# Kernel tuning notes

Measured on AMD Instinct MI355X. Metric: run time of the kernel, lower is better.

The kernel has to match this reference:

```python
import jax, jax.numpy as jnp
import numpy as np

N_STATIC = 20
N_DYNAMIC = 10
INPUT_DIM = N_STATIC + N_DYNAMIC * 9 + 8  # 118
EMBED = 128
HIDDEN = 1536
HIDDEN2 = 1024
OUT = 128
T = 2048


def setup_inputs() -> dict:
    key = jax.random.key(0)
    ks = jax.random.split(key, 20)
    s = lambda i, shape: jax.random.normal(ks[i], shape, dtype=jnp.float32) * 0.02
    inp = {
        "inputVecs": jax.random.normal(ks[0], (T, INPUT_DIM), dtype=jnp.float32),
        # init_hidden(): randn(num_layers, 1, hidden_dim) -> stored as [2, H]
        "h0": jax.random.normal(ks[1], (2, HIDDEN), dtype=jnp.float32),
        "c0": jax.random.normal(ks[2], (2, HIDDEN), dtype=jnp.float32),
        # LSTM layer 0 (input = INPUT_DIM + EMBED)
        "W_ih0": s(3, (4 * HIDDEN, INPUT_DIM + EMBED)),
        "W_hh0": s(4, (4 * HIDDEN, HIDDEN)),
        "b_ih0": s(5, (4 * HIDDEN,)),
        "b_hh0": s(6, (4 * HIDDEN,)),
        # LSTM layer 1
        "W_ih1": s(7, (4 * HIDDEN, HIDDEN)),
        "W_hh1": s(8, (4 * HIDDEN, HIDDEN)),
        "b_ih1": s(9, (4 * HIDDEN,)),
        "b_hh1": s(10, (4 * HIDDEN,)),
        # hiddenLinear: hidden_dim -> hidden2
        "W_hl": s(11, (HIDDEN2, HIDDEN)),
        "b_hl": s(12, (HIDDEN2,)),
        # linear: hidden2 -> output_dim
        "W_out": s(13, (OUT, HIDDEN2)),
        "b_out": s(14, (OUT,)),
        # map: output_dim -> embed_size
        "W_map": s(15, (EMBED, OUT)),
        "b_map": s(16, (EMBED,)),
    }
    return inp


def _lstm_cell(x, h, c, W_ih, W_hh, b_ih, b_hh):
    # torch gate order: i, f, g, o
    gates = W_ih @ x + b_ih + W_hh @ h + b_hh
    i, f, g, o = jnp.split(gates, 4)
    i = jax.nn.sigmoid(i)
    f = jax.nn.sigmoid(f)
    g = jnp.tanh(g)
    o = jax.nn.sigmoid(o)
    c_new = f * c + i * g
    h_new = o * jnp.tanh(c_new)
    return h_new, c_new


def reference(inputVecs, h0, c0, W_ih0, W_hh0, b_ih0, b_hh0,
              W_ih1, W_hh1, b_ih1, b_hh1,
              W_hl, b_hl, W_out, b_out, W_map, b_map):
    embed0 = jnp.zeros((EMBED,), dtype=inputVecs.dtype)

    def step(carry, x):
        h, c, emb = carry  # h,c: [2, H]; emb: [EMBED]
        xt = jnp.concatenate([x, emb])
        h0n, c0n = _lstm_cell(xt, h[0], c[0], W_ih0, W_hh0, b_ih0, b_hh0)
        h1n, c1n = _lstm_cell(h0n, h[1], c[1], W_ih1, W_hh1, b_ih1, b_hh1)
        # dropout p=0 -> identity; two stacked linears (no nonlinearity, faithful)
        y = W_out @ (W_hl @ h1n + b_hl) + b_out
        y = jax.nn.softmax(y)
        emb_new = W_map @ y + b_map
        return (jnp.stack([h0n, h1n]), jnp.stack([c0n, c1n]), emb_new), y

    _, outputs = jax.lax.scan(step, (h0, c0, embed0), inputVecs)
    return outputs  # [T, OUT]
```

## Files before the change

### kernel.cpp

```cpp
#include <hip/hip_runtime.h>
#include <math.h>
#include <stdint.h>

#define T_STEPS 2048
#define XDIM 118
#define EMBD 128
#define HD 1536
#define NA 96
#define NB 128
#define NBLK (NA + NB + 1)

#define EP_A   0
#define EP_B   128
#define EP_C   256
#define EP_AG  288
#define EP_N   320

#define SMEM_BYTES 160032

struct Params {
  const float *x, *h0in, *c0in;
  const float *Wih0, *Whh0, *bih0, *bhh0;
  const float *Wih1, *Whh1, *bih1, *bhh1;
  const float *Whl, *bhl, *Wout, *bout, *Wmap, *bmap;
  float *PRE, *Wc, *bc, *h0buf, *h1buf, *embbuf, *PART;
  uint32_t *ep;
  float *out;
};

__device__ __forceinline__ float bf_lo(uint32_t u){ return __uint_as_float(u << 16); }
__device__ __forceinline__ float bf_hi(uint32_t u){ return __uint_as_float(u & 0xffff0000u); }
__device__ __forceinline__ uint32_t packbf(float a, float b){
  uint32_t ua = __float_as_uint(a), ub = __float_as_uint(b);
  ua = (ua + 0x7fffu + ((ua >> 16) & 1u)) >> 16;
  ub = (ub + 0x7fffu + ((ub >> 16) & 1u)) & 0xffff0000u;
  return (ua & 0xffffu) | ub;
}
__device__ __forceinline__ float gload(const float* p){
  return __hip_atomic_load(p, __ATOMIC_RELAXED, __HIP_MEMORY_SCOPE_AGENT);
}
__device__ __forceinline__ void gstore(float* p, float v){
  __hip_atomic_store(p, v, __ATOMIC_RELAXED, __HIP_MEMORY_SCOPE_AGENT);
}
__device__ __forceinline__ uint32_t gloadu(const uint32_t* p){
  return __hip_atomic_load(p, __ATOMIC_RELAXED, __HIP_MEMORY_SCOPE_AGENT);
}
__device__ __forceinline__ void gstoreu(uint32_t* p, uint32_t v){
  __hip_atomic_store(p, v, __ATOMIC_RELAXED, __HIP_MEMORY_SCOPE_AGENT);
}
__device__ __forceinline__ float sigm(float x){ return 1.f / (1.f + __expf(-x)); }

__device__ __forceinline__ float asrc(const Params& P, int r, int k){
  if (k < HD) return P.Whh0[(size_t)r * HD + k];
  return P.Wih0[(size_t)r * (XDIM + EMBD) + XDIM + (k - HD)];
}
__device__ void run_A(const Params& P, int bid, uint32_t* smem){
  const int tid = threadIdx.x;
  const int w = tid >> 6, l = tid & 63;
  const int O = bid * 16 + w;
  float* xv = (float*)smem;
  uint2* wl2 = (uint2*)(smem + 1664);
  uint32_t wr[4][8];
  uint32_t wremb[4];
#pragma unroll
  for (int g = 0; g < 4; ++g){
    int r = g * HD + O;
#pragma unroll
    for (int p = 0; p < 8; ++p)
      wr[g][p] = packbf(asrc(P, r, 128 * p + 2 * l), asrc(P, r, 128 * p + 2 * l + 1));
#pragma unroll
    for (int q = 0; q < 2; ++q){
      uint2 u;
      u.x = packbf(asrc(P, r, 128 * (8 + 2 * q) + 2 * l), asrc(P, r, 128 * (8 + 2 * q) + 2 * l + 1));
      u.y = packbf(asrc(P, r, 128 * (9 + 2 * q) + 2 * l), asrc(P, r, 128 * (9 + 2 * q) + 2 * l + 1));
      wl2[(q * 4 + g) * 1024 + tid] = u;
    }
    wremb[g] = packbf(asrc(P, r, 1536 + 2 * l), asrc(P, r, 1537 + 2 * l));
  }
  float cst = P.c0in[O];
  int alive = 1;
  __syncthreads();
  for (int t = 0; t < T_STEPS; ++t){
    const float* pre = P.PRE + (size_t)t * 6144;
    float q0 = pre[O], q1 = pre[HD + O], q2 = pre[2 * HD + O], q3 = pre[3 * HD + O];
    if (w == 0 && alive){
      uint32_t n = 0;
      while (gloadu(P.ep + EP_AG) < (uint32_t)t){
        if (++n > 5000000u){ alive = 0; break; }
      }
    }
    __syncthreads();
    const float* hp = P.h0buf + (((t & 1) ^ 1) * HD);
    xv[tid] = gload(hp + tid);
    if (tid < 512) xv[1024 + tid] = gload(hp + 1024 + tid);
    __syncthreads();
    float a0 = 0.f, a1 = 0.f, a2 = 0.f, a3 = 0.f;
#pragma unroll
    for (int p = 0; p < 8; ++p){
      float2 x2 = *(const float2*)&xv[128 * p + 2 * l];
      uint32_t u0 = wr[0][p], u1 = wr[1][p], u2 = wr[2][p], u3 = wr[3][p];
      a0 += bf_lo(u0) * x2.x + bf_hi(u0) * x2.y;
      a1 += bf_lo(u1) * x2.x + bf_hi(u1) * x2.y;
      a2 += bf_lo(u2) * x2.x + bf_hi(u2) * x2.y;
      a3 += bf_lo(u3) * x2.x + bf_hi(u3) * x2.y;
    }
#pragma unroll
    for (int q = 0; q < 2; ++q){
      float2 xa = *(const float2*)&xv[128 * (8 + 2 * q) + 2 * l];
      float2 xb = *(const float2*)&xv[128 * (9 + 2 * q) + 2 * l];
      uint2 u0 = wl2[(q * 4 + 0) * 1024 + tid];
      uint2 u1 = wl2[(q * 4 + 1) * 1024 + tid];
      uint2 u2 = wl2[(q * 4 + 2) * 1024 + tid];
      uint2 u3 = wl2[(q * 4 + 3) * 1024 + tid];
      a0 += bf_lo(u0.x) * xa.x + bf_hi(u0.x) * xa.y + bf_lo(u0.y) * xb.x + bf_hi(u0.y) * xb.y;
      a1 += bf_lo(u1.x) * xa.x + bf_hi(u1.x) * xa.y + bf_lo(u1.y) * xb.x + bf_hi(u1.y) * xb.y;
      a2 += bf_lo(u2.x) * xa.x + bf_hi(u2.x) * xa.y + bf_lo(u2.y) * xb.x + bf_hi(u2.y) * xb.y;
      a3 += bf_lo(u3.x) * xa.x + bf_hi(u3.x) * xa.y + bf_lo(u3.y) * xb.x + bf_hi(u3.y) * xb.y;
    }
    if (w == 0 && alive){
      uint32_t n = 0;
      while (gloadu(P.ep + EP_C) < (uint32_t)t){
        if (++n > 5000000u){ alive = 0; break; }
      }
    }
    __syncthreads();
    if (tid < EMBD) xv[HD + tid] = gload(P.embbuf + (((t & 1) ^ 1) * EMBD) + tid);
    __syncthreads();
    {
      float2 x2 = *(const float2*)&xv[1536 + 2 * l];
      a0 += bf_lo(wremb[0]) * x2.x + bf_hi(wremb[0]) * x2.y;
      a1 += bf_lo(wremb[1]) * x2.x + bf_hi(wremb[1]) * x2.y;
      a2 += bf_lo(wremb[2]) * x2.x + bf_hi(wremb[2]) * x2.y;
      a3 += bf_lo(wremb[3]) * x2.x + bf_hi(wremb[3]) * x2.y;
    }
#pragma unroll
    for (int m = 1; m < 64; m <<= 1){
      a0 += __shfl_xor(a0, m, 64);
      a1 += __shfl_xor(a1, m, 64);
      a2 += __shfl_xor(a2, m, 64);
      a3 += __shfl_xor(a3, m, 64);
    }
    float gi = sigm(a0 + q0);
    float gf = sigm(a1 + q1);
    float gg = tanhf(a2 + q2);
    float go = sigm(a3 + q3);
    cst = gf * cst + gi * gg;
    float hn = go * tanhf(cst);
    if (l == 0) gstore(P.h0buf + (t & 1) * HD + O, hn);
    __syncthreads();
    if (tid == 0) gstoreu(P.ep + EP_A + bid, (uint32_t)(t + 1));
  }
}

__device__ __forceinline__ float bsrc(const Params& P, int r, int k){
  if (k < HD) return P.Wih1[(size_t)r * HD + k];
  return P.Whh1[(size_t)r * HD + (k - HD)];
}
__device__ void run_B(const Params& P, int bidb, uint32_t* smem){
  const int tid = threadIdx.x;
  const int w = tid >> 6, l = tid & 63;
  const int base = bidb * 12;
  float* xv = (float*)smem;
  uint2* wl2 = (uint2*)(smem + 3072);
  float* g1lds = (float*)(smem + 39936);
  float* c1lds = g1lds + 48;
  float* h1lds = c1lds + 12;
  uint32_t wr[3][12];
  float bias[3];
#pragma unroll
  for (int jj = 0; jj < 3; ++jj){
    int idx = 3 * w + jj;
    int g = idx / 12, o = idx % 12;
    int r = g * HD + base + o;
    bias[jj] = P.bih1[r] + P.bhh1[r];
#pragma unroll
    for (int p = 0; p < 12; ++p)
      wr[jj][p] = packbf(bsrc(P, r, 128 * p + 2 * l), bsrc(P, r, 128 * p + 2 * l + 1));
#pragma unroll
    for (int q = 0; q < 6; ++q){
      uint2 u;
      u.x = packbf(bsrc(P, r, 128 * (12 + 2 * q) + 2 * l), bsrc(P, r, 128 * (12 + 2 * q) + 2 * l + 1));
      u.y = packbf(bsrc(P, r, 128 * (13 + 2 * q) + 2 * l), bsrc(P, r, 128 * (13 + 2 * q) + 2 * l + 1));
      wl2[(q * 3 + jj) * 1024 + tid] = u;
    }
  }
  const int jrow = tid >> 2, cpart = tid & 3;
  float wc0 = 0.f, wc1 = 0.f, wc2 = 0.f;
  if (tid < 512){
    const float* wcp = P.Wc + (size_t)jrow * HD + base + cpart * 3;
    wc0 = wcp[0]; wc1 = wcp[1]; wc2 = wcp[2];
  }
  if (tid < 12) c1lds[tid] = P.c0in[HD + base + tid];
  int alive = 1;
  __syncthreads();
  for (int t = 0; t < T_STEPS; ++t){
    if (w == 0 && alive){
      uint32_t n = 0;
      while (gloadu(P.ep + EP_C) < (uint32_t)t){
        if (++n > 5000000u){ alive = 0; break; }
      }
    }
    __syncthreads();
    const float* h1p = P.h1buf + (((t & 1) ^ 1) * HD);
    xv[1536 + tid] = gload(h1p + tid);
    if (tid < 512) xv[2560 + tid] = gload(h1p + 1024 + tid);
    __syncthreads();
    float a0 = 0.f, a1 = 0.f, a2 = 0.f;
#pragma unroll
    for (int q = 0; q < 6; ++q){
      float2 xa = *(const float2*)&xv[128 * (12 + 2 * q) + 2 * l];
      float2 xb = *(const float2*)&xv[128 * (13 + 2 * q) + 2 * l];
      uint2 u0 = wl2[(q * 3 + 0) * 1024 + tid];
      uint2 u1 = wl2[(q * 3 + 1) * 1024 + tid];
      uint2 u2 = wl2[(q * 3 + 2) * 1024 + tid];
      a0 += bf_lo(u0.x) * xa.x + bf_hi(u0.x) * xa.y + bf_lo(u0.y) * xb.x + bf_hi(u0.y) * xb.y;
      a1 += bf_lo(u1.x) * xa.x + bf_hi(u1.x) * xa.y + bf_lo(u1.y) * xb.x + bf_hi(u1.y) * xb.y;
      a2 += bf_lo(u2.x) * xa.x + bf_hi(u2.x) * xa.y + bf_lo(u2.y) * xb.x + bf_hi(u2.y) * xb.y;
    }
    if (w == 0 && alive){
      uint32_t tgt = (uint32_t)(t + 1), n = 0;
      if (bidb == 0){
        while (1){
          uint32_t v0 = gloadu(P.ep + EP_A + l);
          uint32_t v1 = (l < 32) ? gloadu(P.ep + EP_A + 64 + l) : tgt;
          if (__all(v0 >= tgt && v1 >= tgt)) break;
          if (++n > 5000000u){ alive = 0; break; }
        }
        if (l == 0 && alive) gstoreu(P.ep + EP_AG, tgt);
      } else {
        while (gloadu(P.ep + EP_AG) < tgt){
          if (++n > 5000000u){ alive = 0; break; }
        }
      }
    }
    __syncthreads();
    const float* h0p = P.h0buf + (t & 1) * HD;
    xv[tid] = gload(h0p + tid);
    if (tid < 512) xv[1024 + tid] = gload(h0p + 1024 + tid);
    __syncthreads();
#pragma unroll
    for (int p = 0; p < 12; ++p){
      float2 x2 = *(const float2*)&xv[128 * p + 2 * l];
      uint32_t u0 = wr[0][p], u1 = wr[1][p], u2 = wr[2][p];
      a0 += bf_lo(u0) * x2.x + bf_hi(u0) * x2.y;
      a1 += bf_lo(u1) * x2.x + bf_hi(u1) * x2.y;
      a2 += bf_lo(u2) * x2.x + bf_hi(u2) * x2.y;
    }
#pragma unroll
    for (int m = 1; m < 64; m <<= 1){
      a0 += __shfl_xor(a0, m, 64);
      a1 += __shfl_xor(a1, m, 64);
      a2 += __shfl_xor(a2, m, 64);
    }
    if (l == 0){
      g1lds[3 * w + 0] = a0 + bias[0];
      g1lds[3 * w + 1] = a1 + bias[1];
      g1lds[3 * w + 2] = a2 + bias[2];
    }
    __syncthreads();
    if (tid < 12){
      int o = tid;
      float gi = sigm(g1lds[o]);
      float gf = sigm(g1lds[12 + o]);
      float gg = tanhf(g1lds[24 + o]);
      float go = sigm(g1lds[36 + o]);
      float c = gf * c1lds[o] + gi * gg;
      c1lds[o] = c;
      float hn = go * tanhf(c);
      h1lds[o] = hn;
      gstore(P.h1buf + (t & 1) * HD + base + o, hn);
    }
    __syncthreads();
    if (tid < 512){
      float pp = wc0 * h1lds[cpart * 3] + wc1 * h1lds[cpart * 3 + 1] + wc2 * h1lds[cpart * 3 + 2];
      pp += __shfl_xor(pp, 1, 64);
      pp += __shfl_xor(pp, 2, 64);
      if (cpart == 0) gstore(P.PART + bidb * 128 + jrow, pp);
    }
    __syncthreads();
    if (tid == 0) gstoreu(P.ep + EP_B + bidb, (uint32_t)(t + 1));
  }
}

__device__ void run_C(const Params& P, uint32_t* smem){
  const int tid = threadIdx.x;
  float* partred = (float*)smem;
  float* lg   = (float*)(smem + 1024);
  float* plds = (float*)(smem + 1152);
  float* bcs  = (float*)(smem + 1280);
  float* red2 = (float*)(smem + 1408);
  float wm[16];
  const int e = tid >> 3, jc = tid & 7;
#pragma unroll
  for (int i = 0; i < 16; ++i) wm[i] = P.Wmap[(size_t)e * 128 + jc * 16 + i];
  float bm = P.bmap[e];
  if (tid < 128) bcs[tid] = P.bc[tid];
  int alive = 1;
  const int w = tid >> 6, l = tid & 63;
  __syncthreads();
  for (int t = 0; t < T_STEPS; ++t){
    if (w == 0 && alive){
      uint32_t tgt = (uint32_t)(t + 1), n = 0;
      while (1){
        uint32_t v0 = gloadu(P.ep + EP_B + l);
        uint32_t v1 = gloadu(P.ep + EP_B + 64 + l);
        if (__all(v0 >= tgt && v1 >= tgt)) break;
        if (++n > 5000000u){ alive = 0; break; }
      }
    }
    __syncthreads();
    const int j = tid & 127, b8 = tid >> 7;
    float s = 0.f;
#pragma unroll
    for (int i = 0; i < 16; ++i) s += gload(P.PART + (b8 * 16 + i) * 128 + j);
    partred[b8 * 128 + j] = s;
    __syncthreads();
    if (tid < 128){
      float lt = bcs[tid];
#pragma unroll
      for (int i = 0; i < 8; ++i) lt += partred[i * 128 + tid];
      lg[tid] = lt;
    }
    __syncthreads();
    if (tid < 64){
      float m = fmaxf(lg[tid], lg[tid + 64]);
#pragma unroll
      for (int k = 1; k < 64; k <<= 1) m = fmaxf(m, __shfl_xor(m, k, 64));
      float sd = __expf(lg[tid] - m) + __expf(lg[tid + 64] - m);
#pragma unroll
      for (int k = 1; k < 64; k <<= 1) sd += __shfl_xor(sd, k, 64);
      if (tid == 0){ red2[0] = m; red2[1] = 1.f / sd; }
    }
    __syncthreads();
    if (tid < 128){
      float pv = __expf(lg[tid] - red2[0]) * red2[1];
      plds[tid] = pv;
      P.out[(size_t)t * 128 + tid] = pv;
    }
    __syncthreads();
    float a = 0.f;
#pragma unroll
    for (int i = 0; i < 16; ++i) a += wm[i] * plds[jc * 16 + i];
    a += __shfl_xor(a, 1, 64);
    a += __shfl_xor(a, 2, 64);
    a += __shfl_xor(a, 4, 64);
    if (jc == 0) gstore(P.embbuf + (t & 1) * EMBD + e, a + bm);
    __syncthreads();
    if (tid == 0) gstoreu(P.ep + EP_C, (uint32_t)(t + 1));
  }
}

__global__ __launch_bounds__(1024) void k_lstm(Params P){
  extern __shared__ __align__(16) uint32_t smem[];
  int bid = blockIdx.x;
  if (bid < NA) run_A(P, bid, smem);
  else if (bid < NA + NB) run_B(P, bid - NA, smem);
  else run_C(P, smem);
}

__global__ void k_init(const float* h0in, float* h0buf, float* h1buf, float* embbuf,
                       uint32_t* ep){
  int tid = threadIdx.x;
  for (int i = tid; i < HD; i += 256){
    float a = h0in[i], b = h0in[HD + i];
    h0buf[i] = a; h0buf[HD + i] = a;
    h1buf[i] = b; h1buf[HD + i] = b;
  }
  if (tid < 128){ embbuf[tid] = 0.f; embbuf[128 + tid] = 0.f; }
  for (int i = tid; i < EP_N; i += 256) ep[i] = 0u;
}

__global__ void k_pre(const float* x, const float* Wih0, const float* bih0, const float* bhh0, float* PRE){
  int tb = blockIdx.x >> 2;
  int rc = blockIdx.x & 3;
  int tid = threadIdx.x;
  __shared__ float xl[32 * XDIM];
  for (int i = tid; i < 32 * XDIM; i += 256){
    int tt = i / XDIM, k = i % XDIM;
    xl[i] = x[(size_t)(tb * 32 + tt) * XDIM + k];
  }
  __syncthreads();
  for (int rr = 0; rr < 6; ++rr){
    int r = rc * HD + rr * 256 + tid;
    float acc[32];
#pragma unroll
    for (int t = 0; t < 32; ++t) acc[t] = 0.f;
    const float* wrow = Wih0 + (size_t)r * (XDIM + EMBD);
    for (int k = 0; k < XDIM; ++k){
      float wv = wrow[k];
#pragma unroll
      for (int t = 0; t < 32; ++t) acc[t] += wv * xl[t * XDIM + k];
    }
    float bb = bih0[r] + bhh0[r];
    for (int t = 0; t < 32; ++t)
      PRE[(size_t)(tb * 32 + t) * 6144 + r] = acc[t] + bb;
  }
}

__global__ void k_wc(const float* Whl, const float* Wout, const float* bhl, const float* bout,
                     float* Wc, float* bc){
  if (blockIdx.x == 96){
    int j = threadIdx.x;
    if (j < 128){
      float a = 0.f;
      for (int m = 0; m < 1024; ++m) a += Wout[(size_t)j * 1024 + m] * bhl[m];
      bc[j] = a + bout[j];
    }
    return;
  }
  int kt = blockIdx.x % 6, jt = blockIdx.x / 6;
  __shared__ float wo[8 * 1024];
  int tid = threadIdx.x;
  for (int i = tid; i < 8 * 1024; i += 256) wo[i] = Wout[(size_t)(jt * 8) * 1024 + i];
  __syncthreads();
  int k = kt * 256 + tid;
  float acc[8];
#pragma unroll
  for (int jj = 0; jj < 8; ++jj) acc[jj] = 0.f;
  for (int m = 0; m < 1024; ++m){
    float wl = Whl[(size_t)m * HD + k];
#pragma unroll
    for (int jj = 0; jj < 8; ++jj) acc[jj] += wo[jj * 1024 + m] * wl;
  }
#pragma unroll
  for (int jj = 0; jj < 8; ++jj) Wc[(size_t)(jt * 8 + jj) * HD + k] = acc[jj];
}

__global__ void k_sentinel(float* out){ out[0] = 1.0e6f; }

extern "C" void kernel_launch(void* const* d_in, const int* in_sizes, int n_in,
                              void* d_out, int out_size, void* d_ws, size_t ws_size,
                              hipStream_t stream){
  (void)in_sizes; (void)n_in; (void)out_size;
  const float* x    = (const float*)d_in[0];
  const float* h0in = (const float*)d_in[1];
  const float* c0in = (const float*)d_in[2];
  const float* Wih0 = (const float*)d_in[3];
  const float* Whh0 = (const float*)d_in[4];
  const float* bih0 = (const float*)d_in[5];
  const float* bhh0 = (const float*)d_in[6];
  const float* Wih1 = (const float*)d_in[7];
  const float* Whh1 = (const float*)d_in[8];
  const float* bih1 = (const float*)d_in[9];
  const float* bhh1 = (const float*)d_in[10];
  const float* Whl  = (const float*)d_in[11];
  const float* bhl  = (const float*)d_in[12];
  const float* Wout = (const float*)d_in[13];
  const float* bout = (const float*)d_in[14];
  const float* Wmap = (const float*)d_in[15];
  const float* bmap = (const float*)d_in[16];
  float* out = (float*)d_out;
  float* ws = (float*)d_ws;

  size_t off = 0;
  float* PRE    = ws + off; off += (size_t)T_STEPS * 6144;
  float* Wc     = ws + off; off += 128 * HD;
  float* bc     = ws + off; off += 128;
  float* h0buf  = ws + off; off += 2 * HD;
  float* h1buf  = ws + off; off += 2 * HD;
  float* embbuf = ws + off; off += 2 * EMBD;
  float* PART   = ws + off; off += 128 * 128;
  off = (off + 63) & ~(size_t)63;
  uint32_t* ep  = (uint32_t*)(ws + off); off += EP_N;

  if (ws_size < off * sizeof(float) + 1024){
    hipLaunchKernelGGL(k_sentinel, dim3(1), dim3(1), 0, stream, out);
    return;
  }

  (void)hipFuncSetAttribute(reinterpret_cast<const void*>(k_lstm),
                            hipFuncAttributeMaxDynamicSharedMemorySize, SMEM_BYTES);

  hipLaunchKernelGGL(k_init, dim3(1), dim3(256), 0, stream, h0in, h0buf, h1buf, embbuf, ep);
  hipLaunchKernelGGL(k_pre, dim3(256), dim3(256), 0, stream, x, Wih0, bih0, bhh0, PRE);
  hipLaunchKernelGGL(k_wc, dim3(97), dim3(256), 0, stream, Whl, Wout, bhl, bout, Wc, bc);

  Params P;
  P.x = x; P.h0in = h0in; P.c0in = c0in;
  P.Wih0 = Wih0; P.Whh0 = Whh0; P.bih0 = bih0; P.bhh0 = bhh0;
  P.Wih1 = Wih1; P.Whh1 = Whh1; P.bih1 = bih1; P.bhh1 = bhh1;
  P.Whl = Whl; P.bhl = bhl; P.Wout = Wout; P.bout = bout; P.Wmap = Wmap; P.bmap = bmap;
  P.PRE = PRE; P.Wc = Wc; P.bc = bc;
  P.h0buf = h0buf; P.h1buf = h1buf; P.embbuf = embbuf; P.PART = PART;
  P.ep = ep; P.out = out;

  hipLaunchKernelGGL(k_lstm, dim3(NBLK), dim3(1024), SMEM_BYTES, stream, P);
}
```

Before: 33.43 ms.

## Fold embedding map into layer-0 weights and replace block barriers with LDS flags

Precomputes Wfold = Wih0_emb·Wmap and bfold = Wih0_emb·bmap, folding bfold into PRE for t>0. Layer-0 blocks can then consume the softmax output y directly, which removes the map matvec and one stage from the serial per-step chain. Intra-block __syncthreads waits are replaced by an LDS flag that wave 0 sets after polling global counters. Layer-0 blocks now poll all EP_A counters themselves instead of relying on an aggregated flag from block B0, and the softmax is done by a single wave. This shortens the per-step critical path, at the cost of extra bf16 rounding in the folded weights and more fragile spin-wait synchronisation.

```diff
diff --git a/kernel.cpp b/kernel.cpp
--- a/kernel.cpp
+++ b/kernel.cpp
@@ -13,17 +13,17 @@
 #define EP_A   0
 #define EP_B   128
 #define EP_C   256
-#define EP_AG  288
 #define EP_N   320
 
-#define SMEM_BYTES 160032
+#define SMEM_BYTES 160048
 
 struct Params {
   const float *x, *h0in, *c0in;
   const float *Wih0, *Whh0, *bih0, *bhh0;
   const float *Wih1, *Whh1, *bih1, *bhh1;
-  const float *Whl, *bhl, *Wout, *bout, *Wmap, *bmap;
-  float *PRE, *Wc, *bc, *h0buf, *h1buf, *embbuf, *PART;
+  const float *Whl, *bhl, *Wout, *bout;
+  const float *Wfold;
+  float *PRE, *Wc, *bc, *h0buf, *h1buf, *ybuf, *PART;
   uint32_t *ep;
   float *out;
 };
@@ -50,6 +50,17 @@
 }
 __device__ __forceinline__ float sigm(float x){ return 1.f / (1.f + __expf(-x)); }
 
+__device__ __forceinline__ void lds_set(volatile uint32_t* f, uint32_t v){
+  asm volatile("" ::: "memory");
+  *f = v;
+  asm volatile("" ::: "memory");
+}
+__device__ __forceinline__ void lds_wait(volatile uint32_t* f, uint32_t tgt){
+  uint32_t n = 0;
+  while (*f < tgt){ if (++n > 1000000000u) break; }
+  asm volatile("" ::: "memory");
+}
+
 __device__ __forceinline__ float asrc(const Params& P, int r, int k){
   if (k < HD) return P.Whh0[(size_t)r * HD + k];
   return P.Wih0[(size_t)r * (XDIM + EMBD) + XDIM + (k - HD)];
@@ -60,8 +71,9 @@
   const int O = bid * 16 + w;
   float* xv = (float*)smem;
   uint2* wl2 = (uint2*)(smem + 1664);
+  volatile uint32_t* flg = smem + 18048;
   uint32_t wr[4][8];
-  uint32_t wremb[4];
+  uint32_t wry[4];
 #pragma unroll
   for (int g = 0; g < 4; ++g){
     int r = g * HD + O;
@@ -75,21 +87,29 @@
       u.y = packbf(asrc(P, r, 128 * (9 + 2 * q) + 2 * l), asrc(P, r, 128 * (9 + 2 * q) + 2 * l + 1));
       wl2[(q * 4 + g) * 1024 + tid] = u;
     }
-    wremb[g] = packbf(asrc(P, r, 1536 + 2 * l), asrc(P, r, 1537 + 2 * l));
+    wry[g] = packbf(P.Wfold[(size_t)r * 128 + 2 * l], P.Wfold[(size_t)r * 128 + 2 * l + 1]);
   }
   float cst = P.c0in[O];
   int alive = 1;
+  if (tid < 2) flg[tid] = 0u;
   __syncthreads();
   for (int t = 0; t < T_STEPS; ++t){
     const float* pre = P.PRE + (size_t)t * 6144;
     float q0 = pre[O], q1 = pre[HD + O], q2 = pre[2 * HD + O], q3 = pre[3 * HD + O];
-    if (w == 0 && alive){
-      uint32_t n = 0;
-      while (gloadu(P.ep + EP_AG) < (uint32_t)t){
-        if (++n > 5000000u){ alive = 0; break; }
-      }
-    }
-    __syncthreads();
+    if (w == 0){
+      if (alive && t > 0){
+        uint32_t n = 0;
+        while (1){
+          uint32_t v0 = gloadu(P.ep + EP_A + l);
+          uint32_t v1 = (l < 32) ? gloadu(P.ep + EP_A + 64 + l) : (uint32_t)t;
+          if (__all(v0 >= (uint32_t)t && v1 >= (uint32_t)t)) break;
+          if (++n > 5000000u){ alive = 0; break; }
+        }
+      }
+      if (l == 0) lds_set(flg + 0, (uint32_t)t);
+    } else {
+      lds_wait(flg + 0, (uint32_t)t);
+    }
     const float* hp = P.h0buf + (((t & 1) ^ 1) * HD);
     xv[tid] = gload(hp + tid);
     if (tid < 512) xv[1024 + tid] = gload(hp + 1024 + tid);
@@ -117,21 +137,24 @@
       a2 += bf_lo(u2.x) * xa.x + bf_hi(u2.x) * xa.y + bf_lo(u2.y) * xb.x + bf_hi(u2.y) * xb.y;
       a3 += bf_lo(u3.x) * xa.x + bf_hi(u3.x) * xa.y + bf_lo(u3.y) * xb.x + bf_hi(u3.y) * xb.y;
     }
-    if (w == 0 && alive){
-      uint32_t n = 0;
-      while (gloadu(P.ep + EP_C) < (uint32_t)t){
-        if (++n > 5000000u){ alive = 0; break; }
-      }
-    }
-    __syncthreads();
-    if (tid < EMBD) xv[HD + tid] = gload(P.embbuf + (((t & 1) ^ 1) * EMBD) + tid);
-    __syncthreads();
+    if (w == 0){
+      if (alive && t > 0){
+        uint32_t n = 0;
+        while (gloadu(P.ep + EP_C) < (uint32_t)t){
+          if (++n > 5000000u){ alive = 0; break; }
+        }
+      }
+      if (l == 0) lds_set(flg + 1, (uint32_t)t);
+    } else {
+      lds_wait(flg + 1, (uint32_t)t);
+    }
     {
-      float2 x2 = *(const float2*)&xv[1536 + 2 * l];
-      a0 += bf_lo(wremb[0]) * x2.x + bf_hi(wremb[0]) * x2.y;
-      a1 += bf_lo(wremb[1]) * x2.x + bf_hi(wremb[1]) * x2.y;
-      a2 += bf_lo(wremb[2]) * x2.x + bf_hi(wremb[2]) * x2.y;
-      a3 += bf_lo(wremb[3]) * x2.x + bf_hi(wremb[3]) * x2.y;
+      const float* yb = P.ybuf + (((t & 1) ^ 1) * EMBD) + 2 * l;
+      float yx = gload(yb), yy = gload(yb + 1);
+      a0 += bf_lo(wry[0]) * yx + bf_hi(wry[0]) * yy;
+      a1 += bf_lo(wry[1]) * yx + bf_hi(wry[1]) * yy;
+      a2 += bf_lo(wry[2]) * yx + bf_hi(wry[2]) * yy;
+      a3 += bf_lo(wry[3]) * yx + bf_hi(wry[3]) * yy;
     }
 #pragma unroll
     for (int m = 1; m < 64; m <<= 1){
@@ -162,9 +185,9 @@
   const int base = bidb * 12;
   float* xv = (float*)smem;
   uint2* wl2 = (uint2*)(smem + 3072);
-  float* g1lds = (float*)(smem + 39936);
-  float* c1lds = g1lds + 48;
-  float* h1lds = c1lds + 12;
+  float* g1 = (float*)(smem + 39936);
+  float* c1 = g1 + 48;
+  volatile uint32_t* flg = smem + 40008;
   uint32_t wr[3][12];
   float bias[3];
 #pragma unroll
@@ -190,17 +213,22 @@
     const float* wcp = P.Wc + (size_t)jrow * HD + base + cpart * 3;
     wc0 = wcp[0]; wc1 = wcp[1]; wc2 = wcp[2];
   }
-  if (tid < 12) c1lds[tid] = P.c0in[HD + base + tid];
+  if (tid < 12) c1[12 + tid] = P.c0in[HD + base + tid];
+  if (tid < 2) flg[tid] = 0u;
   int alive = 1;
   __syncthreads();
   for (int t = 0; t < T_STEPS; ++t){
-    if (w == 0 && alive){
-      uint32_t n = 0;
-      while (gloadu(P.ep + EP_C) < (uint32_t)t){
-        if (++n > 5000000u){ alive = 0; break; }
-      }
-    }
-    __syncthreads();
+    if (w == 0){
+      if (alive && t > 0){
+        uint32_t n = 0;
+        while (gloadu(P.ep + EP_C) < (uint32_t)t){
+          if (++n > 5000000u){ alive = 0; break; }
+        }
+      }
+      if (l == 0) lds_set(flg + 0, (uint32_t)t);
+    } else {
+      lds_wait(flg + 0, (uint32_t)t);
+    }
     const float* h1p = P.h1buf + (((t & 1) ^ 1) * HD);
     xv[1536 + tid] = gload(h1p + tid);
     if (tid < 512) xv[2560 + tid] = gload(h1p + 1024 + tid);
@@ -217,23 +245,21 @@
       a1 += bf_lo(u1.x) * xa.x + bf_hi(u1.x) * xa.y + bf_lo(u1.y) * xb.x + bf_hi(u1.y) * xb.y;
       a2 += bf_lo(u2.x) * xa.x + bf_hi(u2.x) * xa.y + bf_lo(u2.y) * xb.x + bf_hi(u2.y) * xb.y;
     }
-    if (w == 0 && alive){
-      uint32_t tgt = (uint32_t)(t + 1), n = 0;
-      if (bidb == 0){
+    if (w == 0){
+      uint32_t tgt = (uint32_t)(t + 1);
+      if (alive){
+        uint32_t n = 0;
         while (1){
           uint32_t v0 = gloadu(P.ep + EP_A + l);
           uint32_t v1 = (l < 32) ? gloadu(P.ep + EP_A + 64 + l) : tgt;
           if (__all(v0 >= tgt && v1 >= tgt)) break;
           if (++n > 5000000u){ alive = 0; break; }
         }
-        if (l == 0 && alive) gstoreu(P.ep + EP_AG, tgt);
-      } else {
-        while (gloadu(P.ep + EP_AG) < tgt){
-          if (++n > 5000000u){ alive = 0; break; }
-        }
-      }
-    }
-    __syncthreads();
+      }
+      if (l == 0) lds_set(flg + 1, tgt);
+    } else {
+      lds_wait(flg + 1, (uint32_t)(t + 1));
+    }
     const float* h0p = P.h0buf + (t & 1) * HD;
     xv[tid] = gload(h0p + tid);
     if (tid < 512) xv[1024 + tid] = gload(h0p + 1024 + tid);
@@ -253,29 +279,37 @@
       a2 += __shfl_xor(a2, m, 64);
     }
     if (l == 0){
-      g1lds[3 * w + 0] = a0 + bias[0];
-      g1lds[3 * w + 1] = a1 + bias[1];
-      g1lds[3 * w + 2] = a2 + bias[2];
-    }
-    __syncthreads();
-    if (tid < 12){
-      int o = tid;
-      float gi = sigm(g1lds[o]);
-      float gf = sigm(g1lds[12 + o]);
-      float gg = tanhf(g1lds[24 + o]);
-      float go = sigm(g1lds[36 + o]);
-      float c = gf * c1lds[o] + gi * gg;
-      c1lds[o] = c;
-      float hn = go * tanhf(c);
-      h1lds[o] = hn;
-      gstore(P.h1buf + (t & 1) * HD + base + o, hn);
-    }
-    __syncthreads();
+      g1[3 * w + 0] = a0 + bias[0];
+      g1[3 * w + 1] = a1 + bias[1];
+      g1[3 * w + 2] = a2 + bias[2];
+    }
+    __syncthreads();
+    const int par = ((t & 1) ^ 1) * 12, cur = (t & 1) * 12;
     if (tid < 512){
-      float pp = wc0 * h1lds[cpart * 3] + wc1 * h1lds[cpart * 3 + 1] + wc2 * h1lds[cpart * 3 + 2];
+      float h[3], cc[3];
+#pragma unroll
+      for (int ii = 0; ii < 3; ++ii){
+        int o = cpart * 3 + ii;
+        float gi = sigm(g1[o]);
+        float gf = sigm(g1[12 + o]);
+        float gg = tanhf(g1[24 + o]);
+        float go = sigm(g1[36 + o]);
+        float c = gf * c1[par + o] + gi * gg;
+        cc[ii] = c;
+        h[ii] = go * tanhf(c);
+      }
+      float pp = wc0 * h[0] + wc1 * h[1] + wc2 * h[2];
       pp += __shfl_xor(pp, 1, 64);
       pp += __shfl_xor(pp, 2, 64);
       if (cpart == 0) gstore(P.PART + bidb * 128 + jrow, pp);
+      if (jrow == 0){
+#pragma unroll
+        for (int ii = 0; ii < 3; ++ii){
+          int o = cpart * 3 + ii;
+          c1[cur + o] = cc[ii];
+          gstore(P.h1buf + (t & 1) * HD + base + o, h[ii]);
+        }
+      }
     }
     __syncthreads();
     if (tid == 0) gstoreu(P.ep + EP_B + bidb, (uint32_t)(t + 1));
@@ -285,68 +319,58 @@
 __device__ void run_C(const Params& P, uint32_t* smem){
   const int tid = threadIdx.x;
   float* partred = (float*)smem;
-  float* lg   = (float*)(smem + 1024);
-  float* plds = (float*)(smem + 1152);
-  float* bcs  = (float*)(smem + 1280);
-  float* red2 = (float*)(smem + 1408);
-  float wm[16];
-  const int e = tid >> 3, jc = tid & 7;
-#pragma unroll
-  for (int i = 0; i < 16; ++i) wm[i] = P.Wmap[(size_t)e * 128 + jc * 16 + i];
-  float bm = P.bmap[e];
+  float* bcs = (float*)(smem + 1024);
+  volatile uint32_t* flg = smem + 1152;
+  const int w = tid >> 6, l = tid & 63;
   if (tid < 128) bcs[tid] = P.bc[tid];
+  if (tid == 0) flg[0] = 0u;
   int alive = 1;
-  const int w = tid >> 6, l = tid & 63;
   __syncthreads();
   for (int t = 0; t < T_STEPS; ++t){
-    if (w == 0 && alive){
-      uint32_t tgt = (uint32_t)(t + 1), n = 0;
-      while (1){
-        uint32_t v0 = gloadu(P.ep + EP_B + l);
-        uint32_t v1 = gloadu(P.ep + EP_B + 64 + l);
-        if (__all(v0 >= tgt && v1 >= tgt)) break;
-        if (++n > 5000000u){ alive = 0; break; }
-      }
-    }
-    __syncthreads();
+    uint32_t tgt = (uint32_t)(t + 1);
+    if (w == 0){
+      if (alive){
+        uint32_t n = 0;
+        while (1){
+          uint32_t v0 = gloadu(P.ep + EP_B + l);
+          uint32_t v1 = gloadu(P.ep + EP_B + 64 + l);
+          if (__all(v0 >= tgt && v1 >= tgt)) break;
+          if (++n > 5000000u){ alive = 0; break; }
+        }
+      }
+      if (l == 0) lds_set(flg, tgt);
+    } else {
+      lds_wait(flg, tgt);
+    }
     const int j = tid & 127, b8 = tid >> 7;
     float s = 0.f;
 #pragma unroll
     for (int i = 0; i < 16; ++i) s += gload(P.PART + (b8 * 16 + i) * 128 + j);
     partred[b8 * 128 + j] = s;
     __syncthreads();
-    if (tid < 128){
-      float lt = bcs[tid];
-#pragma unroll
-      for (int i = 0; i < 8; ++i) lt += partred[i * 128 + tid];
-      lg[tid] = lt;
-    }
-    __syncthreads();
-    if (tid < 64){
-      float m = fmaxf(lg[tid], lg[tid + 64]);
+    if (w == 0){
+      float lt0 = bcs[l], lt1 = bcs[64 + l];
+#pragma unroll
+      for (int i = 0; i < 8; ++i){
+        lt0 += partred[i * 128 + l];
+        lt1 += partred[i * 128 + 64 + l];
+      }
+      float m = fmaxf(lt0, lt1);
 #pragma unroll
       for (int k = 1; k < 64; k <<= 1) m = fmaxf(m, __shfl_xor(m, k, 64));
-      float sd = __expf(lg[tid] - m) + __expf(lg[tid + 64] - m);
+      float e0 = __expf(lt0 - m), e1 = __expf(lt1 - m);
+      float sd = e0 + e1;
 #pragma unroll
       for (int k = 1; k < 64; k <<= 1) sd += __shfl_xor(sd, k, 64);
-      if (tid == 0){ red2[0] = m; red2[1] = 1.f / sd; }
-    }
-    __syncthreads();
-    if (tid < 128){
-      float pv = __expf(lg[tid] - red2[0]) * red2[1];
-      plds[tid] = pv;
-      P.out[(size_t)t * 128 + tid] = pv;
-    }
-    __syncthreads();
-    float a = 0.f;
-#pragma unroll
-    for (int i = 0; i < 16; ++i) a += wm[i] * plds[jc * 16 + i];
-    a += __shfl_xor(a, 1, 64);
-    a += __shfl_xor(a, 2, 64);
-    a += __shfl_xor(a, 4, 64);
-    if (jc == 0) gstore(P.embbuf + (t & 1) * EMBD + e, a + bm);
-    __syncthreads();
-    if (tid == 0) gstoreu(P.ep + EP_C, (uint32_t)(t + 1));
+      float inv = 1.f / sd;
+      float p0 = e0 * inv, p1 = e1 * inv;
+      P.out[(size_t)t * 128 + l] = p0;
+      P.out[(size_t)t * 128 + 64 + l] = p1;
+      gstore(P.ybuf + (t & 1) * EMBD + l, p0);
+      gstore(P.ybuf + (t & 1) * EMBD + 64 + l, p1);
+      if (l == 0)
+        __hip_atomic_store(P.ep + EP_C, tgt, __ATOMIC_RELEASE, __HIP_MEMORY_SCOPE_AGENT);
+    }
   }
 }
 
@@ -358,7 +382,7 @@
   else run_C(P, smem);
 }
 
-__global__ void k_init(const float* h0in, float* h0buf, float* h1buf, float* embbuf,
+__global__ void k_init(const float* h0in, float* h0buf, float* h1buf, float* ybuf,
                        uint32_t* ep){
   int tid = threadIdx.x;
   for (int i = tid; i < HD; i += 256){
@@ -366,11 +390,40 @@
     h0buf[i] = a; h0buf[HD + i] = a;
     h1buf[i] = b; h1buf[HD + i] = b;
   }
-  if (tid < 128){ embbuf[tid] = 0.f; embbuf[128 + tid] = 0.f; }
+  if (tid < 128){ ybuf[tid] = 0.f; ybuf[128 + tid] = 0.f; }
   for (int i = tid; i < EP_N; i += 256) ep[i] = 0u;
 }
 
-__global__ void k_pre(const float* x, const float* Wih0, const float* bih0, const float* bhh0, float* PRE){
+__global__ void k_fold(const float* Wih0, const float* Wmap, const float* bmap,
+                       float* Wfold, float* bfold){
+  __shared__ float we[64 * 128];
+  int b = blockIdx.x, tid = threadIdx.x;
+  int r0 = b * 64;
+  for (int i = tid; i < 64 * 128; i += 256){
+    int rr = i >> 7, e = i & 127;
+    we[i] = Wih0[(size_t)(r0 + rr) * (XDIM + EMBD) + XDIM + e];
+  }
+  __syncthreads();
+  int j = tid & 127, half = tid >> 7;
+  float acc[32];
+#pragma unroll
+  for (int rr = 0; rr < 32; ++rr) acc[rr] = 0.f;
+  for (int e = 0; e < 128; ++e){
+    float wv = Wmap[(size_t)e * 128 + j];
+#pragma unroll
+    for (int rr = 0; rr < 32; ++rr) acc[rr] += we[(half * 32 + rr) * 128 + e] * wv;
+  }
+  for (int rr = 0; rr < 32; ++rr)
+    Wfold[(size_t)(r0 + half * 32 + rr) * 128 + j] = acc[rr];
+  if (tid < 64){
+    float a = 0.f;
+    for (int e = 0; e < 128; ++e) a += we[tid * 128 + e] * bmap[e];
+    bfold[r0 + tid] = a;
+  }
+}
+
+__global__ void k_pre(const float* x, const float* Wih0, const float* bih0, const float* bhh0,
+                      const float* bfold, float* PRE){
   int tb = blockIdx.x >> 2;
   int rc = blockIdx.x & 3;
   int tid = threadIdx.x;
@@ -392,8 +445,9 @@
       for (int t = 0; t < 32; ++t) acc[t] += wv * xl[t * XDIM + k];
     }
     float bb = bih0[r] + bhh0[r];
+    float bf = bfold[r];
     for (int t = 0; t < 32; ++t)
-      PRE[(size_t)(tb * 32 + t) * 6144 + r] = acc[t] + bb;
+      PRE[(size_t)(tb * 32 + t) * 6144 + r] = acc[t] + bb + ((tb * 32 + t) > 0 ? bf : 0.f);
   }
 }
 
@@ -456,9 +510,11 @@
   float* PRE    = ws + off; off += (size_t)T_STEPS * 6144;
   float* Wc     = ws + off; off += 128 * HD;
   float* bc     = ws + off; off += 128;
+  float* Wfold  = ws + off; off += (size_t)6144 * 128;
+  float* bfold  = ws + off; off += 6144;
   float* h0buf  = ws + off; off += 2 * HD;
   float* h1buf  = ws + off; off += 2 * HD;
-  float* embbuf = ws + off; off += 2 * EMBD;
+  float* ybuf   = ws + off; off += 2 * EMBD;
   float* PART   = ws + off; off += 128 * 128;
   off = (off + 63) & ~(size_t)63;
   uint32_t* ep  = (uint32_t*)(ws + off); off += EP_N;
@@ -471,17 +527,19 @@
   (void)hipFuncSetAttribute(reinterpret_cast<const void*>(k_lstm),
                             hipFuncAttributeMaxDynamicSharedMemorySize, SMEM_BYTES);
 
-  hipLaunchKernelGGL(k_init, dim3(1), dim3(256), 0, stream, h0in, h0buf, h1buf, embbuf, ep);
-  hipLaunchKernelGGL(k_pre, dim3(256), dim3(256), 0, stream, x, Wih0, bih0, bhh0, PRE);
+  hipLaunchKernelGGL(k_init, dim3(1), dim3(256), 0, stream, h0in, h0buf, h1buf, ybuf, ep);
+  hipLaunchKernelGGL(k_fold, dim3(96), dim3(256), 0, stream, Wih0, Wmap, bmap, Wfold, bfold);
+  hipLaunchKernelGGL(k_pre, dim3(256), dim3(256), 0, stream, x, Wih0, bih0, bhh0, bfold, PRE);
   hipLaunchKernelGGL(k_wc, dim3(97), dim3(256), 0, stream, Whl, Wout, bhl, bout, Wc, bc);
 
   Params P;
   P.x = x; P.h0in = h0in; P.c0in = c0in;
   P.Wih0 = Wih0; P.Whh0 = Whh0; P.bih0 = bih0; P.bhh0 = bhh0;
   P.Wih1 = Wih1; P.Whh1 = Whh1; P.bih1 = bih1; P.bhh1 = bhh1;
-  P.Whl = Whl; P.bhl = bhl; P.Wout = Wout; P.bout = bout; P.Wmap = Wmap; P.bmap = bmap;
+  P.Whl = Whl; P.bhl = bhl; P.Wout = Wout; P.bout = bout;
+  P.Wfold = Wfold;
   P.PRE = PRE; P.Wc = Wc; P.bc = bc;
-  P.h0buf = h0buf; P.h1buf = h1buf; P.embbuf = embbuf; P.PART = PART;
+  P.h0buf = h0buf; P.h1buf = h1buf; P.ybuf = ybuf; P.PART = PART;
   P.ep = ep; P.out = out;
 
   hipLaunchKernelGGL(k_lstm, dim3(NBLK), dim3(1024), SMEM_BYTES, stream, P);
```

After: 31.74 ms. 1.05x faster.
